# Performance work log

Hardware: AMD Instinct MI355X
Metric: run time of the kernel (lower is better)

The kernel has to match this reference:

```python
import jax, jax.numpy as jnp
import numpy as np

N, H, L, S, E, D = 2, 8, 2048, 2048, 64, 64
C, K, BITS, ITERS = 128, 32, 32, 10
TEMP = 1.0 / np.sqrt(E)  # softmax_temp default 1/sqrt(E)


def setup_inputs() -> dict:
    key = jax.random.key(0)
    k1, k2, k3, k4 = jax.random.split(key, 4)
    return {
        "queries": jax.random.normal(k1, (N, L, H, E), jnp.float32),
        "keys": jax.random.normal(k2, (N, S, H, E), jnp.float32),
        "values": jax.random.normal(k3, (N, S, H, D), jnp.float32),
        "planes": jax.random.normal(k4, (BITS, E + 1), jnp.float32),
    }


def _cluster(bits):
    """K-means (Lloyd) on hamming distance over hash bits. bits: [N,H,L,B] in {0,1}."""
    qsum = bits.sum(-1)  # [N,H,L]
    idx0 = jnp.linspace(0, L - 1, C).astype(jnp.int32)  # deterministic centroid init
    cbits0 = bits[:, :, idx0, :]  # [N,H,C,B]

    def assign(cbits):
        # hamming(x,c) = sum(x) + sum(c) - 2*x.c  for 0/1 bits
        d = qsum[..., None] + cbits.sum(-1)[:, :, None, :] \
            - 2.0 * jnp.einsum('nhlb,nhcb->nhlc', bits, cbits)
        return jnp.argmin(d, -1)  # [N,H,L]

    def body(cbits, _):
        cl = assign(cbits)
        oh = jax.nn.one_hot(cl, C, dtype=bits.dtype)       # [N,H,L,C]
        counts = oh.sum(2)                                  # [N,H,C]
        bs = jnp.einsum('nhlc,nhlb->nhcb', oh, bits)        # per-cluster bit sums
        newc = (2.0 * bs > counts[..., None]).astype(bits.dtype)  # majority vote
        newc = jnp.where(counts[..., None] > 0, newc, cbits)      # keep empty clusters
        return newc, None

    cbits, _ = jax.lax.scan(body, cbits0, None, length=ITERS)
    cl = assign(cbits)
    counts = jax.nn.one_hot(cl, C, dtype=jnp.float32).sum(2)
    return cl, counts


def reference(queries, keys, values, planes):
    q = queries.transpose(0, 2, 1, 3)  # [N,H,L,E]
    k = keys.transpose(0, 2, 1, 3)     # [N,H,S,E]
    v = values.transpose(0, 2, 1, 3)   # [N,H,S,D]

    # LSH hashing of queries
    proj = jnp.einsum('nhle,be->nhlb', q, planes[:, :E]) + planes[:, E]
    bits = (proj > 0).astype(jnp.float32)
    cl, counts = _cluster(bits)  # [N,H,L], [N,H,C]

    sorted_indx = jnp.argsort(cl, axis=-1)
    sorted_cl = jnp.take_along_axis(cl, sorted_indx, -1)
    sq = jnp.take_along_axis(q, sorted_indx[..., None], 2)  # queries sorted by cluster

    # grouped queries = per-cluster mean
    counts_safe = jnp.maximum(counts, 1.0)
    oh = jax.nn.one_hot(cl, C, dtype=q.dtype)
    Qg = jnp.einsum('nhlc,nhle->nhce', oh, q) / counts_safe[..., None]

    # centroid-key dot products and top-k key selection per cluster
    QK = jnp.einsum('nhce,nhse->nhcs', Qg, k)  # [N,H,C,S]
    topk_values, topk = jax.lax.top_k(QK, K)   # [N,H,C,K]

    # bottom-k attention (dense per-cluster, top-k positions zeroed)
    A_full = jax.nn.softmax(TEMP * QK, -1)
    iN = jnp.arange(N)[:, None, None, None]
    iH = jnp.arange(H)[None, :, None, None]
    iC = jnp.arange(C)[None, None, :, None]
    mask = jnp.zeros_like(QK).at[iN, iH, iC, topk].set(1.0)
    A_b = A_full * (1.0 - mask)
    A_bottomk = A_b.sum(-1)                              # [N,H,C]
    Vb_g = jnp.einsum('nhcs,nhsd->nhcd', A_b, v)         # [N,H,C,D]
    Vb = jnp.take_along_axis(Vb_g, sorted_cl[..., None], 2)   # broadcast to queries
    A_bk_q = jnp.take_along_axis(A_bottomk, sorted_cl, 2)     # [N,H,L]

    # exact top-k attention per query
    topk_q = jnp.take_along_axis(topk, sorted_cl[..., None], 2)  # [N,H,L,K]
    gather = jax.vmap(jax.vmap(lambda t, i: t[i]))  # over N,H
    K_sel = gather(k, topk_q)  # [N,H,L,K,E]
    V_sel = gather(v, topk_q)  # [N,H,L,K,D]
    QKs = jnp.einsum('nhle,nhlke->nhlk', sq, K_sel)
    inf_mask = jnp.isinf(topk_values[:, 0, 0, :])  # [N,K] (padding sentinel; all False here)
    QKs = jnp.where(inf_mask[:, None, None, :], -jnp.inf, QKs)
    A_s = jax.nn.softmax(TEMP * QKs, -1) * (1.0 - A_bk_q[..., None])
    Vt = jnp.einsum('nhlk,nhlkd->nhld', A_s, V_sel)

    # combine and undo the cluster sort
    Vs = Vt + Vb
    rev = jnp.argsort(sorted_indx, -1)
    V_new = jnp.take_along_axis(Vs, rev[..., None], 2)
    sparse_index = jnp.take_along_axis(topk_q, rev[..., None], 2)
    A_topk = jnp.take_along_axis(A_s, rev[..., None], 2)
    return V_new.transpose(0, 2, 1, 3), sparse_index, A_topk
```

## Files before the change

kernel.cpp:

```cpp
#include <hip/hip_runtime.h>
#include <math.h>

constexpr int cN = 2, cH = 8, cL = 2048, cS = 2048, cE = 64, cD = 64;
constexpr int cC = 128, cK = 32, cB = 32, cIT = 10;
constexpr int cNH = cN * cH;
constexpr int SK = 8;
constexpr int CHUNK = cS / SK;
constexpr int NT = 16;
constexpr int HW = cC * 33;
constexpr int PARTSZ = 32;
constexpr int SLOTS = 256;
constexpr int NBUF = cIT + 1;

__global__ __launch_bounds__(256)
void k_bits(const float* __restrict__ q, const float* __restrict__ planes,
            unsigned int* __restrict__ bits, int* __restrict__ ghist)
{
    __shared__ float pl[cB * 68];
    int tid = threadIdx.x;
    for (int i = tid; i < cB * (cE + 1); i += 256) {
        int b = i / 65, e = i % 65;
        pl[b * 68 + e] = planes[i];
    }
    {
        const int ZS = NBUF * cNH * HW / 128;
        for (int i = tid; i < ZS; i += 256) ghist[(size_t)blockIdx.x * ZS + i] = 0;
    }
    __syncthreads();
    int idx = blockIdx.x * 256 + tid;
    int l = idx % cL, h = (idx / cL) % cH, n = idx / (cL * cH);
    const float* qr = q + (((size_t)n * cL + l) * cH + h) * cE;
    float qv[cE];
#pragma unroll
    for (int e4 = 0; e4 < cE / 4; ++e4) {
        float4 f = ((const float4*)qr)[e4];
        qv[4*e4+0] = f.x; qv[4*e4+1] = f.y; qv[4*e4+2] = f.z; qv[4*e4+3] = f.w;
    }
    unsigned int w = 0;
    for (int b = 0; b < cB; ++b) {
        const float4* pr = (const float4*)(pl + b * 68);
        float acc = 0.f;
#pragma unroll
        for (int e4 = 0; e4 < cE / 4; ++e4) {
            float4 f = pr[e4];
            acc = fmaf(qv[4*e4+0], f.x, acc);
            acc = fmaf(qv[4*e4+1], f.y, acc);
            acc = fmaf(qv[4*e4+2], f.z, acc);
            acc = fmaf(qv[4*e4+3], f.w, acc);
        }
        acc += pl[b * 68 + 64];
        if (acc > 0.f) w |= (1u << b);
    }
    bits[idx] = w;
}

__global__ __launch_bounds__(128)
void k_lloyd(const unsigned int* __restrict__ bits, int* __restrict__ ghist,
             unsigned int* __restrict__ cents, int* __restrict__ cl,
             int* __restrict__ pcounts, int it)
{
    __shared__ unsigned int scb[cC] __attribute__((aligned(16)));
    __shared__ int hist[HW];
    int tid = threadIdx.x, lane = tid & 63;
    int tile = blockIdx.x & (NT - 1), nh = blockIdx.x / NT;
    if (it == 0) {
        if (tid < cC) {
            int i0 = (int)(((double)tid * 2047.0) / 127.0);
            scb[tid] = bits[(size_t)nh * cL + i0];
        }
    } else {
        const unsigned int* cp = cents + (size_t)(it - 1) * cNH * cC + nh * cC;
        const int* gb = ghist + (size_t)((it - 1) * cNH + nh) * HW;
        if (tid < cC) {
            unsigned int oldc = cp[tid];
            int cnt = gb[4096 + tid];
            if (cnt > 0) {
                unsigned int nw = 0;
#pragma unroll
                for (int b = 0; b < cB; ++b)
                    if (2 * gb[tid * 32 + b] > cnt) nw |= (1u << b);
                oldc = nw;
            }
            scb[tid] = oldc;
        }
    }
    for (int i = tid; i < HW; i += 128) hist[i] = 0;
    int l = tile * 128 + tid;
    unsigned int w = bits[(size_t)nh * cL + l];
    unsigned long long mymb = 0ull;
#pragma unroll
    for (int b = 0; b < cB; ++b) {
        unsigned long long m = __ballot((w >> b) & 1u);
        if ((lane & 31) == b) mymb = m;
    }
    __syncthreads();
    if (tile == 0 && it < cIT && tid < cC)
        cents[(size_t)it * cNH * cC + nh * cC + tid] = scb[tid];
    const uint4* scb4 = (const uint4*)scb;
    int best = 0x7fffffff;
    for (int c4 = 0; c4 < cC / 4; ++c4) {
        uint4 cb = scb4[c4];
        int c = c4 * 4;
        best = min(best, (__popc(w ^ cb.x) << 8) | c);
        best = min(best, (__popc(w ^ cb.y) << 8) | (c + 1));
        best = min(best, (__popc(w ^ cb.z) << 8) | (c + 2));
        best = min(best, (__popc(w ^ cb.w) << 8) | (c + 3));
    }
    int bc = best & 255;
    if (it == cIT) cl[(size_t)nh * cL + l] = bc;
    for (int c = 0; c < cC; ++c) {
        unsigned long long m = __ballot(bc == c);
        if (m) {
            if (lane < cB) {
                int contrib = __popcll(m & mymb);
                if (contrib) atomicAdd(&hist[c * 32 + lane], contrib);
            }
            if (lane == 63) atomicAdd(&hist[4096 + c], __popcll(m));
        }
    }
    __syncthreads();
    int* gb = ghist + (size_t)(it * cNH + nh) * HW;
    for (int i = tid; i < HW; i += 128) {
        int v = hist[i];
        if (v) atomicAdd(&gb[i], v);
    }
    if (it == cIT && tid < cC)
        pcounts[(nh * NT + tile) * cC + tid] = hist[4096 + tid];
}

__global__ __launch_bounds__(128)
void k_fin(const int* __restrict__ ghist, int* __restrict__ counts,
           int* __restrict__ moff, int* __restrict__ sched)
{
    __shared__ int scn[cC];
    int c = threadIdx.x, nh = blockIdx.x;
    const int* gb = ghist + (size_t)(cIT * cNH + nh) * HW;
    int cnt = gb[4096 + c];
    counts[nh * cC + c] = cnt;
    scn[c] = cnt;
    sched[nh * SLOTS + c] = -1;
    sched[nh * SLOTS + 128 + c] = -1;
    __syncthreads();
    if (c == 0) {
        int run = 0, slot = 0;
        for (int i = 0; i < cC; ++i) {
            int v = scn[i];
            moff[nh * cC + i] = run; run += v;
            int np = (v + PARTSZ - 1) / PARTSZ;
            for (int p = 0; p < np; ++p)
                sched[nh * SLOTS + slot++] = i | (p << 8);
        }
    }
}

__global__ __launch_bounds__(128)
void k_rank(const int* __restrict__ cl, const int* __restrict__ pcounts,
            const int* __restrict__ moff, int* __restrict__ mlist)
{
    __shared__ int pre[cC];
    __shared__ int wcnt0[cC];
    int tid = threadIdx.x, lane = tid & 63, wid = tid >> 6;
    int tile = blockIdx.x & (NT - 1), nh = blockIdx.x / NT;
    if (tid < cC) {
        int s = 0;
        for (int t = 0; t < tile; ++t) s += pcounts[(nh * NT + t) * cC + tid];
        pre[tid] = s + moff[nh * cC + tid];
    }
    int l = tile * 128 + tid;
    int bc = cl[(size_t)nh * cL + l];
    unsigned long long ltmask = (1ull << lane) - 1ull;
    int myrank = 0;
    for (int c = 0; c < cC; ++c) {
        unsigned long long m = __ballot(bc == c);
        if (wid == 0 && lane == 0) wcnt0[c] = __popcll(m);
        if (bc == c) myrank = __popcll(m & ltmask);
    }
    __syncthreads();
    int off = pre[bc] + myrank + (wid == 1 ? wcnt0[bc] : 0);
    mlist[(size_t)nh * cL + off] = l;
}

__global__ __launch_bounds__(64)
void k_qg(const float* __restrict__ q, const int* __restrict__ mlist,
          const int* __restrict__ moff, const int* __restrict__ counts,
          float* __restrict__ Qg)
{
    int b = blockIdx.x;
    int nh = b >> 7;
    int h = nh % cH, n = nh / cH;
    int lane = threadIdx.x;
    int off = moff[b];
    int cnt = counts[b];
    const int* ml = mlist + (size_t)nh * cL + off;
    const float* qb = q + ((size_t)n * cL * cH + h) * cE + lane;
    float acc = 0.f;
    int j = 0;
    for (; j + 4 <= cnt; j += 4) {
        int i0 = ml[j], i1 = ml[j + 1], i2 = ml[j + 2], i3 = ml[j + 3];
        float v0 = qb[(size_t)i0 * cH * cE];
        float v1 = qb[(size_t)i1 * cH * cE];
        float v2 = qb[(size_t)i2 * cH * cE];
        float v3 = qb[(size_t)i3 * cH * cE];
        acc += v0; acc += v1; acc += v2; acc += v3;
    }
    for (; j < cnt; ++j) acc += qb[(size_t)ml[j] * cH * cE];
    float cs = (float)(cnt > 0 ? cnt : 1);
    Qg[(size_t)b * cE + lane] = acc / cs;
}

__global__ __launch_bounds__(256)
void k_qk_gemm(const float* __restrict__ key, const float* __restrict__ Qg,
               float* __restrict__ QK)
{
    __shared__ float qgT[cE][cC + 2];
    __shared__ float kT[cE][128 + 2];
    int tid = threadIdx.x;
    int bs = blockIdx.x & 15;
    int nh = blockIdx.x >> 4;
    int h = nh % cH, n = nh / cH;
    const float4* qsrc = (const float4*)(Qg + (size_t)nh * cC * cE);
#pragma unroll
    for (int i = 0; i < 8; ++i) {
        int f = tid + 256 * i;
        int c = f >> 4, e4 = (f & 15) << 2;
        float4 v = qsrc[f];
        qgT[e4+0][c] = v.x; qgT[e4+1][c] = v.y; qgT[e4+2][c] = v.z; qgT[e4+3][c] = v.w;
    }
    const float* kb = key + (size_t)n * cS * cH * cE + (size_t)h * cE;
    int s0 = bs * 128;
#pragma unroll
    for (int i = 0; i < 8; ++i) {
        int f = tid + 256 * i;
        int s = f >> 4, e4 = (f & 15) << 2;
        float4 v = *(const float4*)(kb + (size_t)(s0 + s) * (cH * cE) + e4);
        kT[e4+0][s] = v.x; kT[e4+1][s] = v.y; kT[e4+2][s] = v.z; kT[e4+3][s] = v.w;
    }
    __syncthreads();
    int tx = tid & 15, ty = tid >> 4;
    float acc[8][8];
#pragma unroll
    for (int i = 0; i < 8; ++i)
#pragma unroll
        for (int j = 0; j < 8; ++j) acc[i][j] = 0.f;
    for (int e = 0; e < cE; ++e) {
        float qv[8], kv[8];
#pragma unroll
        for (int i = 0; i < 8; ++i) qv[i] = qgT[e][ty + 16 * i];
#pragma unroll
        for (int j = 0; j < 8; ++j) kv[j] = kT[e][tx + 16 * j];
#pragma unroll
        for (int i = 0; i < 8; ++i)
#pragma unroll
            for (int j = 0; j < 8; ++j)
                acc[i][j] = fmaf(qv[i], kv[j], acc[i][j]);
    }
    float* dst = QK + (size_t)nh * cC * cS + s0;
#pragma unroll
    for (int i = 0; i < 8; ++i)
#pragma unroll
        for (int j = 0; j < 8; ++j)
            dst[(size_t)(ty + 16 * i) * cS + tx + 16 * j] = acc[i][j];
}

__global__ __launch_bounds__(256)
void k_sel(float* __restrict__ QK, int* __restrict__ topk,
           float* __restrict__ abk)
{
    __shared__ int sbins[4 * 257];
    __shared__ int ired[4];
    __shared__ float fred[4];
    __shared__ unsigned skey[cK];
    __shared__ float sval[cK];
    __shared__ int sidx[cK];
    __shared__ int stopk[cK];
    __shared__ int sDig, sRem, scnt;
    __shared__ float sM;
    int tid = threadIdx.x, lane = tid & 63, wid = tid >> 6;
    int b = blockIdx.x;
    float* qrow = QK + (size_t)b * cS;
    float v[8]; unsigned key[8];
#pragma unroll
    for (int j = 0; j < 8; ++j) {
        float f = qrow[tid + j * 256];
        v[j] = f;
        unsigned u = __float_as_uint(f);
        key[j] = (u & 0x80000000u) ? ~u : (u | 0x80000000u);
    }
    if (tid == 0) { sRem = cK; scnt = 0; }
    unsigned pfx = 0;
    for (int pass = 0; pass < 4; ++pass) {
        int sh = 24 - 8 * pass;
        for (int i = tid; i < 4 * 257; i += 256) sbins[i] = 0;
        __syncthreads();
        int rem = sRem;
#pragma unroll
        for (int j = 0; j < 8; ++j) {
            bool cand = (pass == 0) || ((key[j] >> (sh + 8)) == pfx);
            if (cand) atomicAdd(&sbins[wid * 257 + ((key[j] >> sh) & 255)], 1);
        }
        __syncthreads();
        if (wid == 0) {
            int d0 = lane * 4;
            int c0 = sbins[d0] + sbins[257 + d0] + sbins[514 + d0] + sbins[771 + d0];
            int c1 = sbins[d0+1] + sbins[257+d0+1] + sbins[514+d0+1] + sbins[771+d0+1];
            int c2 = sbins[d0+2] + sbins[257+d0+2] + sbins[514+d0+2] + sbins[771+d0+2];
            int c3 = sbins[d0+3] + sbins[257+d0+3] + sbins[514+d0+3] + sbins[771+d0+3];
            int tot = c0 + c1 + c2 + c3;
            int incl = tot;
#pragma unroll
            for (int off = 1; off < 64; off <<= 1) {
                int o = __shfl_down(incl, off);
                if (lane + off < 64) incl += o;
            }
            int sufHi = incl - tot;
            int G3 = sufHi, G2 = sufHi + c3, G1 = G2 + c2, G0 = G1 + c1;
            int hit = -1, hG = 0;
            if (G0 < rem && rem <= G0 + c0) { hit = d0 + 0; hG = G0; }
            if (G1 < rem && rem <= G1 + c1) { hit = d0 + 1; hG = G1; }
            if (G2 < rem && rem <= G2 + c2) { hit = d0 + 2; hG = G2; }
            if (G3 < rem && rem <= G3 + c3) { hit = d0 + 3; hG = G3; }
            unsigned long long m = __ballot(hit >= 0);
            int src = __ffsll((long long)m) - 1;
            int dsel = __shfl(hit, src);
            int Gsel = __shfl(hG, src);
            if (lane == 0) { sDig = dsel; sRem = rem - Gsel; }
        }
        __syncthreads();
        pfx = (pfx << 8) | (unsigned)sDig;
    }
    unsigned T = pfx;
    int need = sRem;
    int myT = 0;
#pragma unroll
    for (int j = 0; j < 8; ++j) myT += (key[j] == T);
#pragma unroll
    for (int off = 1; off < 64; off <<= 1) myT += __shfl_xor(myT, off);
    if (lane == 0) ired[wid] = myT;
    __syncthreads();
    int tieTot = ((ired[0] + ired[1]) + ired[2]) + ired[3];
    int tieCut = 0x7fffffff;
    if (tieTot != need) {
        int last = -1;
        for (int t = 0; t < need; ++t) {
            int mymin = 0x7fffffff;
#pragma unroll
            for (int j = 0; j < 8; ++j) {
                int idx = tid + j * 256;
                if (key[j] == T && idx > last) mymin = min(mymin, idx);
            }
#pragma unroll
            for (int off = 1; off < 64; off <<= 1)
                mymin = min(mymin, __shfl_xor(mymin, off));
            __syncthreads();
            if (lane == 0) ired[wid] = mymin;
            __syncthreads();
            last = min(min(ired[0], ired[1]), min(ired[2], ired[3]));
        }
        tieCut = last;
    }
    __syncthreads();
    int selm = 0;
#pragma unroll
    for (int j = 0; j < 8; ++j) {
        int idx = tid + j * 256;
        bool s_ = (key[j] > T) || (key[j] == T && idx <= tieCut);
        if (s_) {
            int slot = atomicAdd(&scnt, 1);
            skey[slot] = key[j]; sidx[slot] = idx; sval[slot] = v[j];
            selm |= (1 << j);
        }
    }
    __syncthreads();
    if (tid < cK) {
        unsigned kt = skey[tid]; int it = sidx[tid];
        int rank = 0;
#pragma unroll
        for (int j = 0; j < cK; ++j)
            rank += (skey[j] > kt) || (skey[j] == kt && sidx[j] < it);
        stopk[rank] = it;
        if (rank == 0) sM = sval[tid];
    }
    __syncthreads();
    if (tid < cK) topk[(size_t)b * cK + tid] = stopk[tid];
    float M = sM;
    float e8[8]; float ps = 0.f;
#pragma unroll
    for (int j = 0; j < 8; ++j) { e8[j] = expf(0.125f * (v[j] - M)); ps += e8[j]; }
#pragma unroll
    for (int off = 1; off < 64; off <<= 1) ps += __shfl_xor(ps, off);
    if (lane == 0) fred[wid] = ps;
    __syncthreads();
    float den = ((fred[0] + fred[1]) + fred[2]) + fred[3];
    float ab = 0.f;
#pragma unroll
    for (int j = 0; j < 8; ++j) {
        float P = (selm & (1 << j)) ? 0.f : e8[j] / den;
        ab += P;
        qrow[tid + j * 256] = P;
    }
#pragma unroll
    for (int off = 1; off < 64; off <<= 1) ab += __shfl_xor(ab, off);
    __syncthreads();
    if (lane == 0) fred[wid] = ab;
    __syncthreads();
    if (tid == 0) abk[b] = ((fred[0] + fred[1]) + fred[2]) + fred[3];
}

__global__ __launch_bounds__(256)
void k_pv(const float* __restrict__ P, const float* __restrict__ val,
          float* __restrict__ part)
{
    __shared__ float pT[64][64 + 2];
    __shared__ float vT[64][cD + 4];
    int tid = threadIdx.x;
    int ch = blockIdx.x & 1;
    int sk = (blockIdx.x >> 1) & 7;
    int nh = blockIdx.x >> 4;
    int h = nh % cH, n = nh / cH;
    int tx = tid & 15, ty = tid >> 4;
    float acc[4][4];
#pragma unroll
    for (int i = 0; i < 4; ++i)
#pragma unroll
        for (int j = 0; j < 4; ++j) acc[i][j] = 0.f;
    const float* pb = P + ((size_t)nh * cC + ch * 64) * cS;
    const float* vb = val + (size_t)n * cS * cH * cD + (size_t)h * cD;
    for (int sub = 0; sub < CHUNK / 64; ++sub) {
        int s0 = sk * CHUNK + sub * 64;
#pragma unroll
        for (int i = 0; i < 4; ++i) {
            int f = tid + 256 * i;
            int c = f >> 4, s4 = (f & 15) << 2;
            float4 v = *(const float4*)(pb + (size_t)c * cS + s0 + s4);
            pT[c][s4+0] = v.x; pT[c][s4+1] = v.y; pT[c][s4+2] = v.z; pT[c][s4+3] = v.w;
        }
#pragma unroll
        for (int i = 0; i < 4; ++i) {
            int f = tid + 256 * i;
            int ss = f >> 4, d4 = (f & 15) << 2;
            float4 v = *(const float4*)(vb + (size_t)(s0 + ss) * (cH * cD) + d4);
            vT[ss][d4+0] = v.x; vT[ss][d4+1] = v.y; vT[ss][d4+2] = v.z; vT[ss][d4+3] = v.w;
        }
        __syncthreads();
        for (int ss = 0; ss < 64; ++ss) {
            float pv[4];
#pragma unroll
            for (int i = 0; i < 4; ++i) pv[i] = pT[ty + 16 * i][ss];
            float4 vv = *(const float4*)&vT[ss][tx * 4];
#pragma unroll
            for (int i = 0; i < 4; ++i) {
                acc[i][0] = fmaf(pv[i], vv.x, acc[i][0]);
                acc[i][1] = fmaf(pv[i], vv.y, acc[i][1]);
                acc[i][2] = fmaf(pv[i], vv.z, acc[i][2]);
                acc[i][3] = fmaf(pv[i], vv.w, acc[i][3]);
            }
        }
        __syncthreads();
    }
    float* dst = part + (((size_t)sk * cNH + nh) * cC + ch * 64) * cD;
#pragma unroll
    for (int i = 0; i < 4; ++i) {
        float4 o; o.x = acc[i][0]; o.y = acc[i][1]; o.z = acc[i][2]; o.w = acc[i][3];
        *(float4*)(dst + (size_t)(ty + 16 * i) * cD + tx * 4) = o;
    }
}

__global__ __launch_bounds__(256)
void k_red(const float* __restrict__ part, float* __restrict__ vbg)
{
    int i = blockIdx.x * 256 + threadIdx.x;
    float acc = 0.f;
    for (int sk = 0; sk < SK; ++sk) acc += part[(size_t)sk * (cNH * cC * cD) + i];
    vbg[i] = acc;
}

__global__ __launch_bounds__(256)
void k_out(const float* __restrict__ q, const float* __restrict__ key,
           const float* __restrict__ val, const int* __restrict__ mlist,
           const int* __restrict__ moff, const int* __restrict__ counts,
           const float* __restrict__ abk, const float* __restrict__ vbg,
           const int* __restrict__ topk, const int* __restrict__ sched,
           float* __restrict__ out)
{
    __shared__ float vlds[cK][cD + 1];
    __shared__ float aslds[4][cK];
    __shared__ int   st[cK];
    int tid = threadIdx.x, lane = tid & 63, wid = tid >> 6;
    int nh = blockIdx.x >> 8;
    int slot = blockIdx.x & 255;
    int item = sched[nh * SLOTS + slot];
    if (item < 0) return;
    int c = item & 255, part = item >> 8;
    int b = nh * cC + c;
    int h = nh % cH, n = nh / cH;
    if (tid < cK) st[tid] = topk[(size_t)b * cK + tid];
    __syncthreads();
    const float* kb = key + ((size_t)n * cS * cH + h) * cE;
    const float* vb = val + ((size_t)n * cS * cH + h) * cD;
    for (int r = wid; r < cK; r += 4)
        vlds[r][lane] = vb[(size_t)st[r] * cH * cD + lane];
    int k = lane >> 1, hh = lane & 1;
    float4 kreg[8];
    {
        const float* kr = kb + (size_t)st[k] * cH * cE + hh * 32;
#pragma unroll
        for (int j = 0; j < 8; ++j) kreg[j] = ((const float4*)kr)[j];
    }
    __syncthreads();
    int cnt = counts[b];
    int off = moff[b];
    float scale = 1.0f - abk[b];
    float vbgd = vbg[(size_t)b * cD + lane];
    float stf = (lane < cK) ? (float)st[lane] : 0.f;
    const int* ml = mlist + (size_t)nh * cL + off;
    const size_t off1 = (size_t)cN * cL * cH * cD;
    const size_t off2 = off1 + (size_t)cN * cH * cL * cK;
    int mstart = part * PARTSZ;
    int mend = min(mstart + PARTSZ, cnt);
    for (int m = mstart + wid; m < mend; m += 4) {
        int l = ml[m];
        const float* qrow = q + (((size_t)n * cL + l) * cH + h) * cE + hh * 32;
        float4 qf[8];
#pragma unroll
        for (int j = 0; j < 8; ++j) qf[j] = ((const float4*)qrow)[j];
        float partial = 0.f;
#pragma unroll
        for (int j = 0; j < 8; ++j) {
            partial = fmaf(qf[j].x, kreg[j].x, partial);
            partial = fmaf(qf[j].y, kreg[j].y, partial);
            partial = fmaf(qf[j].z, kreg[j].z, partial);
            partial = fmaf(qf[j].w, kreg[j].w, partial);
        }
        float qk = partial + __shfl_xor(partial, 1);
        float M = qk;
#pragma unroll
        for (int o = 2; o < 64; o <<= 1) M = fmaxf(M, __shfl_xor(M, o));
        float ev = expf(0.125f * (qk - M));
        float den = ev;
#pragma unroll
        for (int o = 2; o < 64; o <<= 1) den += __shfl_xor(den, o);
        float as_ = (ev / den) * scale;
        if (!hh) aslds[wid][k] = as_;
        float acc = 0.f;
#pragma unroll
        for (int j = 0; j < cK; ++j)
            acc = fmaf(aslds[wid][j], vlds[j][lane], acc);
        acc += vbgd;
        int qidx = nh * cL + l;
        out[(((size_t)n * cL + l) * cH + h) * cD + lane] = acc;
        if (lane < cK) {
            out[off1 + (size_t)qidx * cK + lane] = stf;
            out[off2 + (size_t)qidx * cK + lane] = aslds[wid][lane];
        }
    }
}

extern "C" void kernel_launch(void* const* d_in, const int* in_sizes, int n_in,
                              void* d_out, int out_size, void* d_ws, size_t ws_size,
                              hipStream_t stream)
{
    (void)in_sizes; (void)n_in; (void)out_size; (void)ws_size;
    const float* q      = (const float*)d_in[0];
    const float* key    = (const float*)d_in[1];
    const float* val    = (const float*)d_in[2];
    const float* planes = (const float*)d_in[3];
    char* w = (char*)d_ws;
    unsigned int* bits = (unsigned int*)w;  w += (size_t)cN * cH * cL * 4;
    int*   cl     = (int*)w;                w += (size_t)cN * cH * cL * 4;
    int*   counts = (int*)w;                w += (size_t)cN * cH * cC * 4;
    float* abk    = (float*)w;              w += (size_t)cN * cH * cC * 4;
    float* Qg     = (float*)w;              w += (size_t)cN * cH * cC * cE * 4;
    float* vbg    = (float*)w;              w += (size_t)cN * cH * cC * cD * 4;
    int*   topkp  = (int*)w;                w += (size_t)cN * cH * cC * cK * 4;
    float* QK     = (float*)w;              w += (size_t)cNH * cC * cS * 4;
    float* part   = (float*)w;              w += (size_t)SK * cNH * cC * cD * 4;
    int*   ghist  = (int*)w;                w += (size_t)NBUF * cNH * HW * 4;
    unsigned int* cents = (unsigned int*)w; w += (size_t)NBUF * cNH * cC * 4;
    int*   pcounts= (int*)w;                w += (size_t)cNH * NT * cC * 4;
    int*   mlist  = (int*)w;                w += (size_t)cNH * cL * 4;
    int*   moff   = (int*)w;                w += (size_t)cNH * cC * 4;
    int*   sched  = (int*)w;                w += (size_t)cNH * SLOTS * 4;
    float* out = (float*)d_out;

    k_bits <<<(cN * cH * cL) / 256, 256, 0, stream>>>(q, planes, bits, ghist);
    for (int it = 0; it <= cIT; ++it)
        k_lloyd <<<cNH * NT, 128, 0, stream>>>(bits, ghist, cents, cl, pcounts, it);
    k_fin  <<<cNH, 128, 0, stream>>>(ghist, counts, moff, sched);
    k_rank <<<cNH * NT, 128, 0, stream>>>(cl, pcounts, moff, mlist);
    k_qg     <<<cNH * cC, 64, 0, stream>>>(q, mlist, moff, counts, Qg);
    k_qk_gemm<<<cNH * 16, 256, 0, stream>>>(key, Qg, QK);
    k_sel    <<<cNH * cC, 256, 0, stream>>>(QK, topkp, abk);
    k_pv     <<<cNH * SK * 2, 256, 0, stream>>>(QK, val, part);
    k_red    <<<(cNH * cC * cD) / 256, 256, 0, stream>>>(part, vbg);
    k_out    <<<cNH * SLOTS, 256, 0, stream>>>(q, key, val, mlist, moff, counts,
                                               abk, vbg, topkp, sched, out);
}
```

Measured before the change: 329.2 us.

## Fold cluster-offset finalization into rank kernel and widen output kernel with query prefetch

Removes the separate k_fin launch. Each k_rank block now rebuilds cluster totals and exclusive offsets from the per-tile partial counts, and tile 0 writes counts, offsets and the output schedule. The output kernel moves from 4 to 8 waves per block, and each wave prefetches the next query row into registers while it computes the current one, to hide gather latency. The cost is redundant prefix work in every rank block, more registers per thread in k_out, and waves that leave early when a partition has few members.

```diff
diff --git a/kernel.cpp b/kernel.cpp
--- a/kernel.cpp
+++ b/kernel.cpp
@@ -129,42 +129,48 @@
 }
 
 __global__ __launch_bounds__(128)
-void k_fin(const int* __restrict__ ghist, int* __restrict__ counts,
-           int* __restrict__ moff, int* __restrict__ sched)
-{
+void k_rank(const int* __restrict__ cl, const int* __restrict__ pcounts,
+            int* __restrict__ counts, int* __restrict__ moff,
+            int* __restrict__ sched, int* __restrict__ mlist)
+{
+    __shared__ int pre[cC];
     __shared__ int scn[cC];
-    int c = threadIdx.x, nh = blockIdx.x;
-    const int* gb = ghist + (size_t)(cIT * cNH + nh) * HW;
-    int cnt = gb[4096 + c];
-    counts[nh * cC + c] = cnt;
-    scn[c] = cnt;
-    sched[nh * SLOTS + c] = -1;
-    sched[nh * SLOTS + 128 + c] = -1;
-    __syncthreads();
-    if (c == 0) {
-        int run = 0, slot = 0;
-        for (int i = 0; i < cC; ++i) {
-            int v = scn[i];
-            moff[nh * cC + i] = run; run += v;
-            int np = (v + PARTSZ - 1) / PARTSZ;
-            for (int p = 0; p < np; ++p)
-                sched[nh * SLOTS + slot++] = i | (p << 8);
-        }
-    }
-}
-
-__global__ __launch_bounds__(128)
-void k_rank(const int* __restrict__ cl, const int* __restrict__ pcounts,
-            const int* __restrict__ moff, int* __restrict__ mlist)
-{
-    __shared__ int pre[cC];
+    __shared__ int sbefore[cC];
     __shared__ int wcnt0[cC];
     int tid = threadIdx.x, lane = tid & 63, wid = tid >> 6;
     int tile = blockIdx.x & (NT - 1), nh = blockIdx.x / NT;
     if (tid < cC) {
-        int s = 0;
-        for (int t = 0; t < tile; ++t) s += pcounts[(nh * NT + t) * cC + tid];
-        pre[tid] = s + moff[nh * cC + tid];
+        int tot = 0, bef = 0;
+        for (int t = 0; t < NT; ++t) {
+            int v = pcounts[(nh * NT + t) * cC + tid];
+            if (t < tile) bef += v;
+            tot += v;
+        }
+        scn[tid] = tot;
+        sbefore[tid] = bef;
+    }
+    __syncthreads();
+    if (tid == 0) {
+        int run = 0;
+        for (int i = 0; i < cC; ++i) { pre[i] = run; run += scn[i]; }
+    }
+    __syncthreads();
+    if (tile == 0) {
+        if (tid < cC) {
+            counts[nh * cC + tid] = scn[tid];
+            moff[nh * cC + tid] = pre[tid];
+        }
+        sched[nh * SLOTS + tid] = -1;
+        sched[nh * SLOTS + 128 + tid] = -1;
+        __syncthreads();
+        if (tid == 0) {
+            int slot = 0;
+            for (int i = 0; i < cC; ++i) {
+                int np = (scn[i] + PARTSZ - 1) / PARTSZ;
+                for (int p = 0; p < np; ++p)
+                    sched[nh * SLOTS + slot++] = i | (p << 8);
+            }
+        }
     }
     int l = tile * 128 + tid;
     int bc = cl[(size_t)nh * cL + l];
@@ -176,7 +182,7 @@
         if (bc == c) myrank = __popcll(m & ltmask);
     }
     __syncthreads();
-    int off = pre[bc] + myrank + (wid == 1 ? wcnt0[bc] : 0);
+    int off = pre[bc] + sbefore[bc] + myrank + (wid == 1 ? wcnt0[bc] : 0);
     mlist[(size_t)nh * cL + off] = l;
 }
 
@@ -474,7 +480,7 @@
     vbg[i] = acc;
 }
 
-__global__ __launch_bounds__(256)
+__global__ __launch_bounds__(512)
 void k_out(const float* __restrict__ q, const float* __restrict__ key,
            const float* __restrict__ val, const int* __restrict__ mlist,
            const int* __restrict__ moff, const int* __restrict__ counts,
@@ -483,7 +489,7 @@
            float* __restrict__ out)
 {
     __shared__ float vlds[cK][cD + 1];
-    __shared__ float aslds[4][cK];
+    __shared__ float aslds[8][cK];
     __shared__ int   st[cK];
     int tid = threadIdx.x, lane = tid & 63, wid = tid >> 6;
     int nh = blockIdx.x >> 8;
@@ -497,7 +503,7 @@
     __syncthreads();
     const float* kb = key + ((size_t)n * cS * cH + h) * cE;
     const float* vb = val + ((size_t)n * cS * cH + h) * cD;
-    for (int r = wid; r < cK; r += 4)
+    for (int r = wid; r < cK; r += 8)
         vlds[r][lane] = vb[(size_t)st[r] * cH * cD + lane];
     int k = lane >> 1, hh = lane & 1;
     float4 kreg[8];
@@ -517,12 +523,22 @@
     const size_t off2 = off1 + (size_t)cN * cH * cL * cK;
     int mstart = part * PARTSZ;
     int mend = min(mstart + PARTSZ, cnt);
-    for (int m = mstart + wid; m < mend; m += 4) {
-        int l = ml[m];
-        const float* qrow = q + (((size_t)n * cL + l) * cH + h) * cE + hh * 32;
-        float4 qf[8];
-#pragma unroll
-        for (int j = 0; j < 8; ++j) qf[j] = ((const float4*)qrow)[j];
+    int mym[4]; int nm = 0;
+    for (int m = mstart + wid; m < mend; m += 8) mym[nm++] = ml[m];
+    if (nm == 0) return;
+    float4 qf[8], qn[8];
+    {
+        const float* q0 = q + (((size_t)n * cL + mym[0]) * cH + h) * cE + hh * 32;
+#pragma unroll
+        for (int j = 0; j < 8; ++j) qf[j] = ((const float4*)q0)[j];
+    }
+    for (int i = 0; i < nm; ++i) {
+        if (i + 1 < nm) {
+            const float* q1 = q + (((size_t)n * cL + mym[i + 1]) * cH + h) * cE + hh * 32;
+#pragma unroll
+            for (int j = 0; j < 8; ++j) qn[j] = ((const float4*)q1)[j];
+        }
+        int l = mym[i];
         float partial = 0.f;
 #pragma unroll
         for (int j = 0; j < 8; ++j) {
@@ -552,6 +568,8 @@
             out[off1 + (size_t)qidx * cK + lane] = stf;
             out[off2 + (size_t)qidx * cK + lane] = aslds[wid][lane];
         }
+#pragma unroll
+        for (int j = 0; j < 8; ++j) qf[j] = qn[j];
     }
 }
 
@@ -585,13 +603,12 @@
     k_bits <<<(cN * cH * cL) / 256, 256, 0, stream>>>(q, planes, bits, ghist);
     for (int it = 0; it <= cIT; ++it)
         k_lloyd <<<cNH * NT, 128, 0, stream>>>(bits, ghist, cents, cl, pcounts, it);
-    k_fin  <<<cNH, 128, 0, stream>>>(ghist, counts, moff, sched);
-    k_rank <<<cNH * NT, 128, 0, stream>>>(cl, pcounts, moff, mlist);
+    k_rank <<<cNH * NT, 128, 0, stream>>>(cl, pcounts, counts, moff, sched, mlist);
     k_qg     <<<cNH * cC, 64, 0, stream>>>(q, mlist, moff, counts, Qg);
     k_qk_gemm<<<cNH * 16, 256, 0, stream>>>(key, Qg, QK);
     k_sel    <<<cNH * cC, 256, 0, stream>>>(QK, topkp, abk);
     k_pv     <<<cNH * SK * 2, 256, 0, stream>>>(QK, val, part);
     k_red    <<<(cNH * cC * cD) / 256, 256, 0, stream>>>(part, vbg);
-    k_out    <<<cNH * SLOTS, 256, 0, stream>>>(q, key, val, mlist, moff, counts,
+    k_out    <<<cNH * SLOTS, 512, 0, stream>>>(q, key, val, mlist, moff, counts,
                                                abk, vbg, topkp, sched, out);
 }
```

After: 357.8 us. 8.7% more time.
